# Kernel tuning notes

Measured on AMD Instinct MI355X. Metric: run time of the kernel, lower is better.

## Reference

```python
import jax, jax.numpy as jnp
import numpy as np

B, S, H, NH, FF, L = 2, 2048, 768, 12, 3072, 2
DH = H // NH
EPS = 1e-12
NEG = -10000.0


def setup_inputs() -> dict:
    key = jax.random.key(0)
    ks = jax.random.split(key, 10)
    w = lambda k, shp: jax.random.normal(k, shp, dtype=jnp.float32) * 0.02
    return {
        'hidden_states': jax.random.normal(ks[0], (B, S, H), dtype=jnp.float32),
        'attention_mask': jnp.ones((B, S), jnp.float32),
        'bias_matrix': jax.random.normal(ks[1], (S, S), dtype=jnp.float32) * 0.1,
        'bias_coef': jnp.ones((), jnp.float32),
        'Wq': w(ks[2], (L, H, H)), 'bq': jnp.zeros((L, H), jnp.float32),
        'Wk': w(ks[3], (L, H, H)), 'bk': jnp.zeros((L, H), jnp.float32),
        'Wv': w(ks[4], (L, H, H)), 'bv': jnp.zeros((L, H), jnp.float32),
        'Wo': w(ks[5], (L, H, H)), 'bo': jnp.zeros((L, H), jnp.float32),
        'ln1_g': jnp.ones((L, H), jnp.float32), 'ln1_b': jnp.zeros((L, H), jnp.float32),
        'Wi': w(ks[6], (L, H, FF)), 'bi': jnp.zeros((L, FF), jnp.float32),
        'Wo2': w(ks[7], (L, FF, H)), 'bo2': jnp.zeros((L, H), jnp.float32),
        'ln2_g': jnp.ones((L, H), jnp.float32), 'ln2_b': jnp.zeros((L, H), jnp.float32),
    }


def _layer_norm(x, g, b):
    mu = jnp.mean(x, axis=-1, keepdims=True)
    var = jnp.mean(jnp.square(x - mu), axis=-1, keepdims=True)
    return (x - mu) * jax.lax.rsqrt(var + EPS) * g + b


def reference(hidden_states, attention_mask, bias_matrix, bias_coef,
              Wq, bq, Wk, bk, Wv, bv, Wo, bo, ln1_g, ln1_b,
              Wi, bi, Wo2, bo2, ln2_g, ln2_b):
    # extended additive mask: [B,1,1,S]
    ext_mask = (1.0 - attention_mask)[:, None, None, :] * NEG
    bias = bias_matrix[None, None] * bias_coef  # [1,1,S,S]
    x = hidden_states
    scale = 1.0 / np.sqrt(DH)
    for i in range(L):
        q = (x @ Wq[i] + bq[i]).reshape(B, S, NH, DH).transpose(0, 2, 1, 3)
        k = (x @ Wk[i] + bk[i]).reshape(B, S, NH, DH).transpose(0, 2, 1, 3)
        v = (x @ Wv[i] + bv[i]).reshape(B, S, NH, DH).transpose(0, 2, 1, 3)
        scores = jnp.einsum('bhqd,bhkd->bhqk', q, k) * scale
        scores = scores + bias + ext_mask
        probs = jax.nn.softmax(scores, axis=-1)  # dropout = identity (eval)
        ctx = jnp.einsum('bhqk,bhkd->bhqd', probs, v)
        ctx = ctx.transpose(0, 2, 1, 3).reshape(B, S, H)
        attn_out = ctx @ Wo[i] + bo[i]
        x = _layer_norm(attn_out + x, ln1_g[i], ln1_b[i])
        inter = jax.nn.gelu(x @ Wi[i] + bi[i], approximate=False)
        ffn_out = inter @ Wo2[i] + bo2[i]
        x = _layer_norm(ffn_out + x, ln2_g[i], ln2_b[i])
    return x
```

## Files before the change

### kernel.cpp

```cpp
#include <hip/hip_runtime.h>
#include <hip/hip_bf16.h>
#include <math.h>

#define BB     2
#define SS     2048
#define HH     768
#define NHEAD  12
#define DHEAD  64
#define FFD    3072
#define NLAYER 2
#define MTOK   (BB*SS)

typedef __attribute__((ext_vector_type(8))) short bf16x8;
typedef __attribute__((ext_vector_type(4))) short bf16x4;
typedef __attribute__((ext_vector_type(4))) float f32x4;

__device__ __forceinline__ short f2bs(float f) {
    union { float f; unsigned u; } v; v.f = f;
    unsigned r = v.u + 0x7FFF + ((v.u >> 16) & 1);
    return (short)(r >> 16);
}
__device__ __forceinline__ float bs2f(short s) {
    union { unsigned u; float f; } v; v.u = ((unsigned)(unsigned short)s) << 16;
    return v.f;
}
__device__ __forceinline__ void gl2lds16(const short* g, short* l) {
    __builtin_amdgcn_global_load_lds(
        (const __attribute__((address_space(1))) unsigned int*)g,
        (__attribute__((address_space(3))) unsigned int*)l, 16, 0, 0);
}

struct TJobs { const float* src[8]; short* dst[8]; };

__global__ __launch_bounds__(256)
void transpose_cvt_batch(TJobs jobs, int K, int N)
{
    const float* __restrict__ W  = jobs.src[blockIdx.z];
    short* __restrict__ Wt = jobs.dst[blockIdx.z];
    __shared__ short tile[32][33];
    const int k0 = blockIdx.x * 32, n0 = blockIdx.y * 32;
    const int tx = threadIdx.x & 31, ty = threadIdx.x >> 5;
#pragma unroll
    for (int i = 0; i < 4; i++)
        tile[ty + i*8][tx] = f2bs(W[(size_t)(k0 + ty + i*8) * N + n0 + tx]);
    __syncthreads();
#pragma unroll
    for (int i = 0; i < 4; i++)
        Wt[(size_t)(n0 + ty + i*8) * K + k0 + tx] = tile[tx][ty + i*8];
}

__global__ __launch_bounds__(256)
void cvt_bf16(const float* __restrict__ src, short* __restrict__ dst, int n)
{
    const int i = blockIdx.x * 256 + threadIdx.x;
    if (i < n) dst[i] = f2bs(src[i]);
}

__global__ __launch_bounds__(256)
void pack_bias(const float* __restrict__ bq, const float* __restrict__ bk,
               const float* __restrict__ bv, float* __restrict__ bqkv)
{
    const int t = blockIdx.x * 256 + threadIdx.x;
    if (t >= NLAYER * 2304) return;
    const int l = t / 2304, r = t % 2304;
    const float* src = (r < 768) ? bq : (r < 1536 ? bk : bv);
    bqkv[t] = src[l*768 + (r % 768)];
}

__global__ __launch_bounds__(256)
void bias_frag_prep(const float* __restrict__ biasM, const float* __restrict__ mask,
                    const float* __restrict__ coefp, short* __restrict__ bFrag)
{
    __shared__ float tile[64][129];
    const int tid = threadIdx.x;
    const int qb = blockIdx.x, q0 = qb*64, k0 = blockIdx.y*128;
#pragma unroll
    for (int p = 0; p < 8; p++) {
        const int row = p*8 + (tid >> 5);
        const int col = (tid & 31) * 4;
        float4 v = *(const float4*)&biasM[(size_t)(q0 + row)*SS + k0 + col];
        tile[row][col+0] = v.x; tile[row][col+1] = v.y;
        tile[row][col+2] = v.z; tile[row][col+3] = v.w;
    }
    __syncthreads();
    const float coef = coefp[0];
    const int lane = tid & 63, w = tid >> 6;
    const int l16 = lane & 15, g = lane >> 4;
    const int qrow = w*16 + l16;
#pragma unroll
    for (int b = 0; b < BB; b++) {
#pragma unroll
        for (int kt = 0; kt < 8; kt++) {
            bf16x4 o;
#pragma unroll
            for (int r = 0; r < 4; r++) {
                const int kk = kt*16 + g*4 + r;
                const float madd = (1.f - mask[b*SS + k0 + kk]) * (-10000.0f);
                o[r] = f2bs(tile[qrow][kk] * coef + madd);
            }
            const size_t idx = ((((size_t)b*32 + qb)*4 + w)*128 + (k0>>4) + kt)*256 + lane*4;
            *(bf16x4*)&bFrag[idx] = o;
        }
    }
}

__global__ __launch_bounds__(256)
void gemm_mfma(const short* __restrict__ A, const short* __restrict__ Bt,
               const float* __restrict__ bias, short* __restrict__ C, int ldc,
               int M, int N, int K, int gelu, short* __restrict__ VtOut, int vsplit)
{
    __shared__ short sA[128*32];
    __shared__ short sB[128*32];
    const int tid  = threadIdx.x;
    const int w    = tid >> 6;
    const int lane = tid & 63;
    const int l16  = lane & 15, g = lane >> 4;
    const int wm   = w & 1, wn = w >> 1;
    const size_t m0 = (size_t)blockIdx.y * 128, n0 = (size_t)blockIdx.x * 128;

    const int srow = lane >> 2;
    const int kc   = lane & 3;

    f32x4 acc[4][4];
#pragma unroll
    for (int i = 0; i < 4; i++)
#pragma unroll
        for (int j = 0; j < 4; j++) acc[i][j] = (f32x4){0.f,0.f,0.f,0.f};

    const short* gA0 = A  + (m0 + w*32 +      srow) * (size_t)K + kc*8;
    const short* gA1 = A  + (m0 + w*32 + 16 + srow) * (size_t)K + kc*8;
    const short* gB0 = Bt + (n0 + w*32 +      srow) * (size_t)K + kc*8;
    const short* gB1 = Bt + (n0 + w*32 + 16 + srow) * (size_t)K + kc*8;
    short* lA0 = &sA[(w*32     )*32];
    short* lA1 = &sA[(w*32 + 16)*32];
    short* lB0 = &sB[(w*32     )*32];
    short* lB1 = &sB[(w*32 + 16)*32];

    for (int k0 = 0; k0 < K; k0 += 32) {
        gl2lds16(gA0 + k0, lA0);
        gl2lds16(gA1 + k0, lA1);
        gl2lds16(gB0 + k0, lB0);
        gl2lds16(gB1 + k0, lB1);
        __syncthreads();

        bf16x8 af[4], bfr[4];
#pragma unroll
        for (int mt = 0; mt < 4; mt++)
            af[mt] = *(const bf16x8*)&sA[(wm*64 + mt*16 + l16)*32 + g*8];
#pragma unroll
        for (int nt = 0; nt < 4; nt++)
            bfr[nt] = *(const bf16x8*)&sB[(wn*64 + nt*16 + l16)*32 + g*8];
#pragma unroll
        for (int mt = 0; mt < 4; mt++)
#pragma unroll
            for (int nt = 0; nt < 4; nt++)
                acc[mt][nt] = __builtin_amdgcn_mfma_f32_16x16x32_bf16(
                                  af[mt], bfr[nt], acc[mt][nt], 0, 0, 0);
        __syncthreads();
    }

#pragma unroll
    for (int mt = 0; mt < 4; mt++) {
        const size_t row0 = m0 + wm*64 + mt*16 + g*4;
#pragma unroll
        for (int nt = 0; nt < 4; nt++) {
            const size_t col = n0 + wn*64 + nt*16 + l16;
            if ((int)col >= vsplit) {
                short4 t;
                t.x = f2bs(acc[mt][nt][0] + bias[col]);
                t.y = f2bs(acc[mt][nt][1] + bias[col]);
                t.z = f2bs(acc[mt][nt][2] + bias[col]);
                t.w = f2bs(acc[mt][nt][3] + bias[col]);
                *(short4*)&VtOut[(size_t)(col - vsplit)*MTOK + row0] = t;
            } else {
#pragma unroll
                for (int r = 0; r < 4; r++) {
                    float v = acc[mt][nt][r] + bias[col];
                    if (gelu) v = 0.5f * v * (1.f + erff(v * 0.70710678118f));
                    C[(row0 + r) * (size_t)ldc + col] = f2bs(v);
                }
            }
        }
    }
}

__global__ __launch_bounds__(256)
void gemm_mfma_n64(const short* __restrict__ A, const short* __restrict__ Bt,
                   const float* __restrict__ bias, short* __restrict__ C, int ldc,
                   int M, int N, int K, int gelu)
{
    __shared__ short sA[128*32];
    __shared__ short sB[64*32];
    const int tid  = threadIdx.x;
    const int w    = tid >> 6;
    const int lane = tid & 63;
    const int l16  = lane & 15, g = lane >> 4;
    const int wm   = w & 1, wn = w >> 1;
    const size_t m0 = (size_t)blockIdx.y * 128, n0 = (size_t)blockIdx.x * 64;

    const int srow = lane >> 2;
    const int kc   = lane & 3;

    f32x4 acc[4][2];
#pragma unroll
    for (int i = 0; i < 4; i++)
#pragma unroll
        for (int j = 0; j < 2; j++) acc[i][j] = (f32x4){0.f,0.f,0.f,0.f};

    const short* gA0 = A  + (m0 + w*32 +      srow) * (size_t)K + kc*8;
    const short* gA1 = A  + (m0 + w*32 + 16 + srow) * (size_t)K + kc*8;
    const short* gB0 = Bt + (n0 + w*16 +      srow) * (size_t)K + kc*8;
    short* lA0 = &sA[(w*32     )*32];
    short* lA1 = &sA[(w*32 + 16)*32];
    short* lB0 = &sB[(w*16     )*32];

    for (int k0 = 0; k0 < K; k0 += 32) {
        gl2lds16(gA0 + k0, lA0);
        gl2lds16(gA1 + k0, lA1);
        gl2lds16(gB0 + k0, lB0);
        __syncthreads();

        bf16x8 af[4], bfr[2];
#pragma unroll
        for (int mt = 0; mt < 4; mt++)
            af[mt] = *(const bf16x8*)&sA[(wm*64 + mt*16 + l16)*32 + g*8];
#pragma unroll
        for (int nt = 0; nt < 2; nt++)
            bfr[nt] = *(const bf16x8*)&sB[(wn*32 + nt*16 + l16)*32 + g*8];
#pragma unroll
        for (int mt = 0; mt < 4; mt++)
#pragma unroll
            for (int nt = 0; nt < 2; nt++)
                acc[mt][nt] = __builtin_amdgcn_mfma_f32_16x16x32_bf16(
                                  af[mt], bfr[nt], acc[mt][nt], 0, 0, 0);
        __syncthreads();
    }

#pragma unroll
    for (int mt = 0; mt < 4; mt++) {
        const size_t row0 = m0 + wm*64 + mt*16 + g*4;
#pragma unroll
        for (int nt = 0; nt < 2; nt++) {
            const size_t col = n0 + wn*32 + nt*16 + l16;
#pragma unroll
            for (int r = 0; r < 4; r++) {
                float v = acc[mt][nt][r] + bias[col];
                if (gelu) v = 0.5f * v * (1.f + erff(v * 0.70710678118f));
                C[(row0 + r) * (size_t)ldc + col] = f2bs(v);
            }
        }
    }
}

__global__ __launch_bounds__(256, 3)
void attn_fused(const short* __restrict__ QK, const short* __restrict__ Vt,
                const short* __restrict__ bFrag, short* __restrict__ CTX)
{
    __shared__ short sK[128*72];
    __shared__ short sV[64*136];
    __shared__ short sP[64*136];

    const int qb  = blockIdx.x;
    const int q0  = qb * 64;
    const int h   = blockIdx.y;
    const int b   = blockIdx.z;
    const int tid = threadIdx.x;
    const int w   = tid >> 6;
    const int lane = tid & 63;
    const int l16 = lane & 15;
    const int g   = lane >> 4;
    const float scale = 0.125f;

    const short* qrow = QK + ((size_t)(b*SS) + q0 + w*16 + l16) * 1536 + h*64;
    bf16x8 bQ0 = *(const bf16x8*)(qrow + g*8);
    bf16x8 bQ1 = *(const bf16x8*)(qrow + 32 + g*8);

    f32x4 O[4];
#pragma unroll
    for (int d = 0; d < 4; d++) O[d] = (f32x4){0.f,0.f,0.f,0.f};
    float m_q = -1e30f, l_q = 0.f;

    const int krow = tid >> 3, kch = tid & 7;
    const int vrow = tid >> 4, vch = tid & 15;
    const short* Kg = QK + ((size_t)(b*SS) + krow)*1536 + 768 + h*64 + kch*8;
    const short* Vg = Vt + ((size_t)(h*64 + vrow))*MTOK + b*SS + vch*8;
    const short* bF = bFrag + ((((size_t)b*32 + qb)*4 + w)*128)*256 + lane*4;

    short* prow = &sP[(w*16 + l16)*136];

    bf16x8 kreg[4], vreg[4];
#pragma unroll
    for (int p = 0; p < 4; p++) {
        kreg[p] = *(const bf16x8*)(Kg + (size_t)(p*32)*1536);
        vreg[p] = *(const bf16x8*)(Vg + (size_t)(p*16)*MTOK);
    }

    for (int k0 = 0; k0 < SS; k0 += 128) {
        const short* bFt = bF + ((size_t)(k0 >> 4))*256;
        bf16x4 bb[8];
#pragma unroll
        for (int t = 0; t < 8; t++)
            bb[t] = *(const bf16x4*)(bFt + (size_t)t*256);

#pragma unroll
        for (int p = 0; p < 4; p++) {
            *(bf16x8*)&sK[(p*32 + krow)*72 + kch*8]   = kreg[p];
            *(bf16x8*)&sV[(p*16 + vrow)*136 + vch*8]  = vreg[p];
        }
        __syncthreads();

        if (k0 + 128 < SS) {
#pragma unroll
            for (int p = 0; p < 4; p++) {
                kreg[p] = *(const bf16x8*)(Kg + (size_t)(k0 + 128 + p*32)*1536);
                vreg[p] = *(const bf16x8*)(Vg + (size_t)(p*16)*MTOK + k0 + 128);
            }
        }

        float S[8][4];
#pragma unroll
        for (int t = 0; t < 8; t++) {
            bf16x8 aK0 = *(const bf16x8*)&sK[(t*16 + l16)*72 + g*8];
            bf16x8 aK1 = *(const bf16x8*)&sK[(t*16 + l16)*72 + 32 + g*8];
            f32x4 c = (f32x4){0.f,0.f,0.f,0.f};
            c = __builtin_amdgcn_mfma_f32_16x16x32_bf16(aK0, bQ0, c, 0, 0, 0);
            c = __builtin_amdgcn_mfma_f32_16x16x32_bf16(aK1, bQ1, c, 0, 0, 0);
#pragma unroll
            for (int r = 0; r < 4; r++)
                S[t][r] = c[r]*scale + bs2f(bb[t][r]);
        }

        float tm[8];
#pragma unroll
        for (int t = 0; t < 8; t++)
            tm[t] = fmaxf(fmaxf(S[t][0], S[t][1]), fmaxf(S[t][2], S[t][3]));
        float mx = fmaxf(fmaxf(fmaxf(tm[0], tm[1]), fmaxf(tm[2], tm[3])),
                         fmaxf(fmaxf(tm[4], tm[5]), fmaxf(tm[6], tm[7])));
        mx = fmaxf(mx, __shfl_xor(mx, 16));
        mx = fmaxf(mx, __shfl_xor(mx, 32));
        const float mnew  = fmaxf(m_q, mx);
        const float alpha = __expf(m_q - mnew);
        float ts[8];
#pragma unroll
        for (int t = 0; t < 8; t++) {
            float p0 = __expf(S[t][0] - mnew);
            float p1 = __expf(S[t][1] - mnew);
            float p2 = __expf(S[t][2] - mnew);
            float p3 = __expf(S[t][3] - mnew);
            S[t][0] = p0; S[t][1] = p1; S[t][2] = p2; S[t][3] = p3;
            ts[t] = (p0 + p1) + (p2 + p3);
        }
        float rs = ((ts[0] + ts[1]) + (ts[2] + ts[3]))
                 + ((ts[4] + ts[5]) + (ts[6] + ts[7]));
        rs += __shfl_xor(rs, 16);
        rs += __shfl_xor(rs, 32);
        l_q = l_q * alpha + rs;
        m_q = mnew;

#pragma unroll
        for (int r = 0; r < 4; r++) {
            const float ar = __shfl(alpha, g*4 + r);
#pragma unroll
            for (int d = 0; d < 4; d++) O[d][r] *= ar;
        }

#pragma unroll
        for (int t = 0; t < 8; t++) {
            unsigned int d0, d1;
            asm("v_cvt_pk_bf16_f32 %0, %1, %2" : "=v"(d0) : "v"(S[t][0]), "v"(S[t][1]));
            asm("v_cvt_pk_bf16_f32 %0, %1, %2" : "=v"(d1) : "v"(S[t][2]), "v"(S[t][3]));
            uint2 u; u.x = d0; u.y = d1;
            *(uint2*)&prow[t*16 + g*4] = u;
        }

#pragma unroll
        for (int hh = 0; hh < 2; hh++) {
            bf16x8 aP0 = *(const bf16x8*)&prow[hh*64 + g*8];
            bf16x8 aP1 = *(const bf16x8*)&prow[hh*64 + 32 + g*8];
#pragma unroll
            for (int d = 0; d < 4; d++) {
                bf16x8 v0 = *(const bf16x8*)&sV[(d*16 + l16)*136 + hh*64 + g*8];
                bf16x8 v1 = *(const bf16x8*)&sV[(d*16 + l16)*136 + hh*64 + 32 + g*8];
                O[d] = __builtin_amdgcn_mfma_f32_16x16x32_bf16(aP0, v0, O[d], 0, 0, 0);
                O[d] = __builtin_amdgcn_mfma_f32_16x16x32_bf16(aP1, v1, O[d], 0, 0, 0);
            }
        }
        __syncthreads();
    }

    float linv[4];
#pragma unroll
    for (int r = 0; r < 4; r++)
        linv[r] = 1.f / __shfl(l_q, g*4 + r);
#pragma unroll
    for (int d = 0; d < 4; d++)
#pragma unroll
        for (int r = 0; r < 4; r++)
            CTX[((size_t)(b*SS) + q0 + w*16 + g*4 + r)*HH + h*64 + d*16 + l16]
                = f2bs(O[d][r] * linv[r]);
}

__global__ __launch_bounds__(256)
void add_ln(const short* __restrict__ A, const short* __restrict__ R,
            const float* __restrict__ g, const float* __restrict__ beta,
            short* __restrict__ Out, float* __restrict__ OutF)
{
    const int lane = threadIdx.x & 63;
    const int row  = blockIdx.x * 4 + (threadIdx.x >> 6);
    const size_t base = (size_t)row * HH;

    float v[12];
    float s = 0.f;
#pragma unroll
    for (int p = 0; p < 3; p++) {
        const int c = p*256 + lane*4;
        bf16x4 av = *(const bf16x4*)&A[base + c];
        bf16x4 rv = *(const bf16x4*)&R[base + c];
#pragma unroll
        for (int j = 0; j < 4; j++) {
            float x = bs2f(av[j]) + bs2f(rv[j]);
            v[p*4 + j] = x;
            s += x;
        }
    }
    s += __shfl_xor(s, 1);  s += __shfl_xor(s, 2);  s += __shfl_xor(s, 4);
    s += __shfl_xor(s, 8);  s += __shfl_xor(s, 16); s += __shfl_xor(s, 32);
    const float mu = s * (1.f / HH);

    float s2 = 0.f;
#pragma unroll
    for (int j = 0; j < 12; j++) { float d = v[j] - mu; s2 += d * d; }
    s2 += __shfl_xor(s2, 1);  s2 += __shfl_xor(s2, 2);  s2 += __shfl_xor(s2, 4);
    s2 += __shfl_xor(s2, 8);  s2 += __shfl_xor(s2, 16); s2 += __shfl_xor(s2, 32);
    const float rstd = rsqrtf(s2 * (1.f / HH) + 1e-12f);

#pragma unroll
    for (int p = 0; p < 3; p++) {
        const int c = p*256 + lane*4;
        float4 gv = *(const float4*)&g[c];
        float4 bv = *(const float4*)&beta[c];
        float o0 = (v[p*4+0] - mu) * rstd * gv.x + bv.x;
        float o1 = (v[p*4+1] - mu) * rstd * gv.y + bv.y;
        float o2 = (v[p*4+2] - mu) * rstd * gv.z + bv.z;
        float o3 = (v[p*4+3] - mu) * rstd * gv.w + bv.w;
        bf16x4 ov; ov[0] = f2bs(o0); ov[1] = f2bs(o1); ov[2] = f2bs(o2); ov[3] = f2bs(o3);
        *(bf16x4*)&Out[base + c] = ov;
        if (OutF) {
            float4 of; of.x = o0; of.y = o1; of.z = o2; of.w = o3;
            *(float4*)&OutF[base + c] = of;
        }
    }
}

extern "C" void kernel_launch(void* const* d_in, const int* in_sizes, int n_in,
                              void* d_out, int out_size, void* d_ws, size_t ws_size,
                              hipStream_t stream)
{
    const float* hs    = (const float*)d_in[0];
    const float* mask  = (const float*)d_in[1];
    const float* biasM = (const float*)d_in[2];
    const float* coef  = (const float*)d_in[3];
    const float* Wq    = (const float*)d_in[4];
    const float* bq    = (const float*)d_in[5];
    const float* Wk    = (const float*)d_in[6];
    const float* bk    = (const float*)d_in[7];
    const float* Wv    = (const float*)d_in[8];
    const float* bv    = (const float*)d_in[9];
    const float* Wo    = (const float*)d_in[10];
    const float* bo    = (const float*)d_in[11];
    const float* ln1g  = (const float*)d_in[12];
    const float* ln1b  = (const float*)d_in[13];
    const float* Wi    = (const float*)d_in[14];
    const float* bi    = (const float*)d_in[15];
    const float* Wo2   = (const float*)d_in[16];
    const float* bo2   = (const float*)d_in[17];
    const float* ln2g  = (const float*)d_in[18];
    const float* ln2b  = (const float*)d_in[19];

    const size_t sH   = (size_t)MTOK * HH;
    const size_t sQK  = (size_t)MTOK * 1536;
    const size_t sVt  = (size_t)HH * MTOK;
    const size_t WPL  = 7077888;
    short* wt    = (short*)d_ws;
    float* bqkv  = (float*)(wt + 2*WPL);
    short* bFrag = (short*)(bqkv + 2*2304);
    short* X     = bFrag + (size_t)2*SS*SS;
    short* X2    = X  + sH;
    short* QK    = X2 + sH;
    short* Vt    = QK + sQK;
    short* CTX   = Vt + sVt;
    short* TMP   = QK;
    short* INTER = QK;
    short* TMP2  = X;

    const dim3 blk(256);

    TJobs jH, jI, jO;
    for (int l = 0; l < NLAYER; l++) {
        short* wl = wt + (size_t)l * WPL;
        jH.src[l*4+0] = Wq + (size_t)l*HH*HH;  jH.dst[l*4+0] = wl;
        jH.src[l*4+1] = Wk + (size_t)l*HH*HH;  jH.dst[l*4+1] = wl + 768*768;
        jH.src[l*4+2] = Wv + (size_t)l*HH*HH;  jH.dst[l*4+2] = wl + 1536*768;
        jH.src[l*4+3] = Wo + (size_t)l*HH*HH;  jH.dst[l*4+3] = wl + 1769472;
        jI.src[l] = Wi  + (size_t)l*HH*FFD;    jI.dst[l] = wl + 2359296;
        jO.src[l] = Wo2 + (size_t)l*FFD*HH;    jO.dst[l] = wl + 4718592;
    }
    transpose_cvt_batch<<<dim3(24,24,8), blk, 0, stream>>>(jH, HH, HH);
    transpose_cvt_batch<<<dim3(24,96,2), blk, 0, stream>>>(jI, HH, FFD);
    transpose_cvt_batch<<<dim3(96,24,2), blk, 0, stream>>>(jO, FFD, HH);
    bias_frag_prep<<<dim3(SS/64, SS/128), blk, 0, stream>>>(biasM, mask, coef, bFrag);
    pack_bias<<<dim3((NLAYER*2304 + 255)/256), blk, 0, stream>>>(bq, bk, bv, bqkv);
    cvt_bf16<<<dim3((int)((sH + 255)/256)), blk, 0, stream>>>(hs, X, (int)sH);

    const dim3 gQKV(2304/128, MTOK/128);
    const dim3 gH64(HH/64,    MTOK/128);
    const dim3 gFF (FFD/128,  MTOK/128);
    const dim3 gA  (SS/64, NHEAD, BB);
    const dim3 gLN (MTOK/4);
    const int NOSPLIT = 1 << 30;

    for (int l = 0; l < NLAYER; l++) {
        short* wl = wt + (size_t)l * WPL;
        gemm_mfma<<<gQKV, blk, 0, stream>>>(X, wl, bqkv + l*2304, QK, 1536,
                                            MTOK, 2304, HH, 0, Vt, 1536);
        attn_fused<<<gA, blk, 0, stream>>>(QK, Vt, bFrag, CTX);
        gemm_mfma_n64<<<gH64, blk, 0, stream>>>(CTX, wl + 1769472, bo + l*HH, TMP, HH,
                                                MTOK, HH, HH, 0);
        add_ln<<<gLN, blk, 0, stream>>>(TMP, X, ln1g + l*HH, ln1b + l*HH, X2, nullptr);
        gemm_mfma<<<gFF, blk, 0, stream>>>(X2, wl + 2359296, bi + l*FFD, INTER, FFD,
                                           MTOK, FFD, HH, 1, nullptr, NOSPLIT);
        gemm_mfma_n64<<<gH64, blk, 0, stream>>>(INTER, wl + 4718592, bo2 + l*HH, TMP2, HH,
                                                MTOK, HH, FFD, 0);
        add_ln<<<gLN, blk, 0, stream>>>(TMP2, X2, ln2g + l*HH, ln2b + l*HH, X,
                                        (l == NLAYER-1) ? (float*)d_out : nullptr);
    }
}
```

Measured before the change: 604.9 us.

## Keep P in registers via permlane swaps, load V directly from global, double-buffer K

The attention kernel no longer stages P and V through shared memory. The softmax probabilities are repacked in registers with v_permlane32/16_swap into the MFMA operand layout, and V fragments are loaded straight from global memory in matching layout, split into two batches to overlap with the softmax math. K tiles are double-buffered in LDS so there is one barrier per iteration. This cuts LDS traffic and footprint, which may allow higher occupancy, but relies on permlane swap semantics being correct and adds global-load latency for V on the critical path.

```diff
diff --git a/kernel.cpp b/kernel.cpp
--- a/kernel.cpp
+++ b/kernel.cpp
@@ -256,9 +256,7 @@
 void attn_fused(const short* __restrict__ QK, const short* __restrict__ Vt,
                 const short* __restrict__ bFrag, short* __restrict__ CTX)
 {
-    __shared__ short sK[128*72];
-    __shared__ short sV[64*136];
-    __shared__ short sP[64*136];
+    __shared__ short sK[2][128*72];
 
     const int qb  = blockIdx.x;
     const int q0  = qb * 64;
@@ -281,53 +279,62 @@
     float m_q = -1e30f, l_q = 0.f;
 
     const int krow = tid >> 3, kch = tid & 7;
-    const int vrow = tid >> 4, vch = tid & 15;
     const short* Kg = QK + ((size_t)(b*SS) + krow)*1536 + 768 + h*64 + kch*8;
-    const short* Vg = Vt + ((size_t)(h*64 + vrow))*MTOK + b*SS + vch*8;
+    const short* Vg = Vt + ((size_t)(h*64 + l16))*MTOK + b*SS + g*8;
     const short* bF = bFrag + ((((size_t)b*32 + qb)*4 + w)*128)*256 + lane*4;
 
-    short* prow = &sP[(w*16 + l16)*136];
-
-    bf16x8 kreg[4], vreg[4];
-#pragma unroll
-    for (int p = 0; p < 4; p++) {
+    bf16x8 kreg[4];
+#pragma unroll
+    for (int p = 0; p < 4; p++)
         kreg[p] = *(const bf16x8*)(Kg + (size_t)(p*32)*1536);
-        vreg[p] = *(const bf16x8*)(Vg + (size_t)(p*16)*MTOK);
-    }
+#pragma unroll
+    for (int p = 0; p < 4; p++)
+        *(bf16x8*)&sK[0][(p*32 + krow)*72 + kch*8] = kreg[p];
+#pragma unroll
+    for (int p = 0; p < 4; p++)
+        kreg[p] = *(const bf16x8*)(Kg + (size_t)(128 + p*32)*1536);
+    __syncthreads();
 
     for (int k0 = 0; k0 < SS; k0 += 128) {
+        const int cur = (k0 >> 7) & 1;
+        const short* sKc = sK[cur];
+
+        if (k0 + 128 < SS) {
+            short* sKn = sK[cur ^ 1];
+#pragma unroll
+            for (int p = 0; p < 4; p++)
+                *(bf16x8*)&sKn[(p*32 + krow)*72 + kch*8] = kreg[p];
+            if (k0 + 256 < SS) {
+#pragma unroll
+                for (int p = 0; p < 4; p++)
+                    kreg[p] = *(const bf16x8*)(Kg + (size_t)(k0 + 256 + p*32)*1536);
+            }
+        }
+
         const short* bFt = bF + ((size_t)(k0 >> 4))*256;
         bf16x4 bb[8];
 #pragma unroll
         for (int t = 0; t < 8; t++)
             bb[t] = *(const bf16x4*)(bFt + (size_t)t*256);
 
-#pragma unroll
-        for (int p = 0; p < 4; p++) {
-            *(bf16x8*)&sK[(p*32 + krow)*72 + kch*8]   = kreg[p];
-            *(bf16x8*)&sV[(p*16 + vrow)*136 + vch*8]  = vreg[p];
-        }
-        __syncthreads();
-
-        if (k0 + 128 < SS) {
-#pragma unroll
-            for (int p = 0; p < 4; p++) {
-                kreg[p] = *(const bf16x8*)(Kg + (size_t)(k0 + 128 + p*32)*1536);
-                vreg[p] = *(const bf16x8*)(Vg + (size_t)(p*16)*MTOK + k0 + 128);
-            }
-        }
-
         float S[8][4];
 #pragma unroll
         for (int t = 0; t < 8; t++) {
-            bf16x8 aK0 = *(const bf16x8*)&sK[(t*16 + l16)*72 + g*8];
-            bf16x8 aK1 = *(const bf16x8*)&sK[(t*16 + l16)*72 + 32 + g*8];
+            bf16x8 aK0 = *(const bf16x8*)&sKc[(t*16 + l16)*72 + g*8];
+            bf16x8 aK1 = *(const bf16x8*)&sKc[(t*16 + l16)*72 + 32 + g*8];
             f32x4 c = (f32x4){0.f,0.f,0.f,0.f};
             c = __builtin_amdgcn_mfma_f32_16x16x32_bf16(aK0, bQ0, c, 0, 0, 0);
             c = __builtin_amdgcn_mfma_f32_16x16x32_bf16(aK1, bQ1, c, 0, 0, 0);
 #pragma unroll
             for (int r = 0; r < 4; r++)
                 S[t][r] = c[r]*scale + bs2f(bb[t][r]);
+        }
+
+        bf16x8 vf0[4], vf1[4];
+#pragma unroll
+        for (int d = 0; d < 4; d++) {
+            vf0[d] = *(const bf16x8*)(Vg + (size_t)(d*16)*MTOK + k0);
+            vf1[d] = *(const bf16x8*)(Vg + (size_t)(d*16)*MTOK + k0 + 32);
         }
 
         float tm[8];
@@ -357,6 +364,13 @@
         l_q = l_q * alpha + rs;
         m_q = mnew;
 
+        bf16x8 vf2[4], vf3[4];
+#pragma unroll
+        for (int d = 0; d < 4; d++) {
+            vf2[d] = *(const bf16x8*)(Vg + (size_t)(d*16)*MTOK + k0 + 64);
+            vf3[d] = *(const bf16x8*)(Vg + (size_t)(d*16)*MTOK + k0 + 96);
+        }
+
 #pragma unroll
         for (int r = 0; r < 4; r++) {
             const float ar = __shfl(alpha, g*4 + r);
@@ -364,27 +378,34 @@
             for (int d = 0; d < 4; d++) O[d][r] *= ar;
         }
 
-#pragma unroll
-        for (int t = 0; t < 8; t++) {
-            unsigned int d0, d1;
-            asm("v_cvt_pk_bf16_f32 %0, %1, %2" : "=v"(d0) : "v"(S[t][0]), "v"(S[t][1]));
-            asm("v_cvt_pk_bf16_f32 %0, %1, %2" : "=v"(d1) : "v"(S[t][2]), "v"(S[t][3]));
-            uint2 u; u.x = d0; u.y = d1;
-            *(uint2*)&prow[t*16 + g*4] = u;
-        }
-
-#pragma unroll
-        for (int hh = 0; hh < 2; hh++) {
-            bf16x8 aP0 = *(const bf16x8*)&prow[hh*64 + g*8];
-            bf16x8 aP1 = *(const bf16x8*)&prow[hh*64 + 32 + g*8];
-#pragma unroll
-            for (int d = 0; d < 4; d++) {
-                bf16x8 v0 = *(const bf16x8*)&sV[(d*16 + l16)*136 + hh*64 + g*8];
-                bf16x8 v1 = *(const bf16x8*)&sV[(d*16 + l16)*136 + hh*64 + 32 + g*8];
-                O[d] = __builtin_amdgcn_mfma_f32_16x16x32_bf16(aP0, v0, O[d], 0, 0, 0);
-                O[d] = __builtin_amdgcn_mfma_f32_16x16x32_bf16(aP1, v1, O[d], 0, 0, 0);
-            }
-        }
+#define PVU(u, vf)                                                             \
+        {                                                                      \
+            unsigned pa, pb, pc, pe;                                           \
+            asm("v_cvt_pk_bf16_f32 %0, %1, %2" : "=v"(pa)                      \
+                : "v"(S[2*(u)][0]),   "v"(S[2*(u)][1]));                       \
+            asm("v_cvt_pk_bf16_f32 %0, %1, %2" : "=v"(pb)                      \
+                : "v"(S[2*(u)][2]),   "v"(S[2*(u)][3]));                       \
+            asm("v_cvt_pk_bf16_f32 %0, %1, %2" : "=v"(pc)                      \
+                : "v"(S[2*(u)+1][0]), "v"(S[2*(u)+1][1]));                     \
+            asm("v_cvt_pk_bf16_f32 %0, %1, %2" : "=v"(pe)                      \
+                : "v"(S[2*(u)+1][2]), "v"(S[2*(u)+1][3]));                     \
+            asm("v_permlane32_swap_b32 %0, %1" : "+v"(pa), "+v"(pc));          \
+            asm("v_permlane16_swap_b32 %0, %1" : "+v"(pa), "+v"(pc));          \
+            asm("v_permlane32_swap_b32 %0, %1" : "+v"(pb), "+v"(pe));          \
+            asm("v_permlane16_swap_b32 %0, %1" : "+v"(pb), "+v"(pe));          \
+            union { unsigned uw[4]; bf16x8 v; } P_;                            \
+            P_.uw[0] = pa; P_.uw[1] = pb; P_.uw[2] = pc; P_.uw[3] = pe;        \
+            _Pragma("unroll")                                                  \
+            for (int d = 0; d < 4; d++)                                        \
+                O[d] = __builtin_amdgcn_mfma_f32_16x16x32_bf16(                \
+                           P_.v, vf[d], O[d], 0, 0, 0);                        \
+        }
+        PVU(0, vf0)
+        PVU(1, vf1)
+        PVU(2, vf2)
+        PVU(3, vf3)
+#undef PVU
+
         __syncthreads();
     }
 
```

Result: slower. 705.6 us (+16.6%).

## Use K=64 tiles in GEMMs and register-permute P for attention PV

Applied to the files above, without the earlier changes.

Both GEMM kernels now stage two 32-wide K slices per iteration into doubled shared buffers, which halves the number of barrier pairs per K sweep at the cost of more LDS per block. The attention kernel no longer writes softmax probabilities to shared memory and reads them back. It converts them to bf16 and rearranges them across lanes with permlane swap instructions to form the MFMA A operand directly. That removes the sP buffer, and the launch bound rises to 4 blocks per CU. The lane permutation has to match the MFMA operand layout exactly, and the higher occupancy target can constrain register allocation.

```diff
diff --git a/kernel.cpp b/kernel.cpp
--- a/kernel.cpp
+++ b/kernel.cpp
@@ -109,8 +109,8 @@
                const float* __restrict__ bias, short* __restrict__ C, int ldc,
                int M, int N, int K, int gelu, short* __restrict__ VtOut, int vsplit)
 {
-    __shared__ short sA[128*32];
-    __shared__ short sB[128*32];
+    __shared__ short sA[2][128*32];
+    __shared__ short sB[2][128*32];
     const int tid  = threadIdx.x;
     const int w    = tid >> 6;
     const int lane = tid & 63;
@@ -131,31 +131,35 @@
     const short* gA1 = A  + (m0 + w*32 + 16 + srow) * (size_t)K + kc*8;
     const short* gB0 = Bt + (n0 + w*32 +      srow) * (size_t)K + kc*8;
     const short* gB1 = Bt + (n0 + w*32 + 16 + srow) * (size_t)K + kc*8;
-    short* lA0 = &sA[(w*32     )*32];
-    short* lA1 = &sA[(w*32 + 16)*32];
-    short* lB0 = &sB[(w*32     )*32];
-    short* lB1 = &sB[(w*32 + 16)*32];
-
-    for (int k0 = 0; k0 < K; k0 += 32) {
-        gl2lds16(gA0 + k0, lA0);
-        gl2lds16(gA1 + k0, lA1);
-        gl2lds16(gB0 + k0, lB0);
-        gl2lds16(gB1 + k0, lB1);
+    const int oA0 = (w*32     )*32, oA1 = (w*32 + 16)*32;
+
+    for (int k0 = 0; k0 < K; k0 += 64) {
+        gl2lds16(gA0 + k0,      &sA[0][oA0]);
+        gl2lds16(gA1 + k0,      &sA[0][oA1]);
+        gl2lds16(gB0 + k0,      &sB[0][oA0]);
+        gl2lds16(gB1 + k0,      &sB[0][oA1]);
+        gl2lds16(gA0 + k0 + 32, &sA[1][oA0]);
+        gl2lds16(gA1 + k0 + 32, &sA[1][oA1]);
+        gl2lds16(gB0 + k0 + 32, &sB[1][oA0]);
+        gl2lds16(gB1 + k0 + 32, &sB[1][oA1]);
         __syncthreads();
 
-        bf16x8 af[4], bfr[4];
-#pragma unroll
-        for (int mt = 0; mt < 4; mt++)
-            af[mt] = *(const bf16x8*)&sA[(wm*64 + mt*16 + l16)*32 + g*8];
-#pragma unroll
-        for (int nt = 0; nt < 4; nt++)
-            bfr[nt] = *(const bf16x8*)&sB[(wn*64 + nt*16 + l16)*32 + g*8];
-#pragma unroll
-        for (int mt = 0; mt < 4; mt++)
+#pragma unroll
+        for (int s = 0; s < 2; s++) {
+            bf16x8 af[4], bfr[4];
+#pragma unroll
+            for (int mt = 0; mt < 4; mt++)
+                af[mt] = *(const bf16x8*)&sA[s][(wm*64 + mt*16 + l16)*32 + g*8];
 #pragma unroll
             for (int nt = 0; nt < 4; nt++)
-                acc[mt][nt] = __builtin_amdgcn_mfma_f32_16x16x32_bf16(
-                                  af[mt], bfr[nt], acc[mt][nt], 0, 0, 0);
+                bfr[nt] = *(const bf16x8*)&sB[s][(wn*64 + nt*16 + l16)*32 + g*8];
+#pragma unroll
+            for (int mt = 0; mt < 4; mt++)
+#pragma unroll
+                for (int nt = 0; nt < 4; nt++)
+                    acc[mt][nt] = __builtin_amdgcn_mfma_f32_16x16x32_bf16(
+                                      af[mt], bfr[nt], acc[mt][nt], 0, 0, 0);
+        }
         __syncthreads();
     }
 
@@ -189,8 +193,8 @@
                    const float* __restrict__ bias, short* __restrict__ C, int ldc,
                    int M, int N, int K, int gelu)
 {
-    __shared__ short sA[128*32];
-    __shared__ short sB[64*32];
+    __shared__ short sA[2][128*32];
+    __shared__ short sB[2][64*32];
     const int tid  = threadIdx.x;
     const int w    = tid >> 6;
     const int lane = tid & 63;
@@ -210,29 +214,33 @@
     const short* gA0 = A  + (m0 + w*32 +      srow) * (size_t)K + kc*8;
     const short* gA1 = A  + (m0 + w*32 + 16 + srow) * (size_t)K + kc*8;
     const short* gB0 = Bt + (n0 + w*16 +      srow) * (size_t)K + kc*8;
-    short* lA0 = &sA[(w*32     )*32];
-    short* lA1 = &sA[(w*32 + 16)*32];
-    short* lB0 = &sB[(w*16     )*32];
-
-    for (int k0 = 0; k0 < K; k0 += 32) {
-        gl2lds16(gA0 + k0, lA0);
-        gl2lds16(gA1 + k0, lA1);
-        gl2lds16(gB0 + k0, lB0);
+    const int oA0 = (w*32     )*32, oA1 = (w*32 + 16)*32, oB0 = (w*16)*32;
+
+    for (int k0 = 0; k0 < K; k0 += 64) {
+        gl2lds16(gA0 + k0,      &sA[0][oA0]);
+        gl2lds16(gA1 + k0,      &sA[0][oA1]);
+        gl2lds16(gB0 + k0,      &sB[0][oB0]);
+        gl2lds16(gA0 + k0 + 32, &sA[1][oA0]);
+        gl2lds16(gA1 + k0 + 32, &sA[1][oA1]);
+        gl2lds16(gB0 + k0 + 32, &sB[1][oB0]);
         __syncthreads();
 
-        bf16x8 af[4], bfr[2];
-#pragma unroll
-        for (int mt = 0; mt < 4; mt++)
-            af[mt] = *(const bf16x8*)&sA[(wm*64 + mt*16 + l16)*32 + g*8];
-#pragma unroll
-        for (int nt = 0; nt < 2; nt++)
-            bfr[nt] = *(const bf16x8*)&sB[(wn*32 + nt*16 + l16)*32 + g*8];
-#pragma unroll
-        for (int mt = 0; mt < 4; mt++)
+#pragma unroll
+        for (int s = 0; s < 2; s++) {
+            bf16x8 af[4], bfr[2];
+#pragma unroll
+            for (int mt = 0; mt < 4; mt++)
+                af[mt] = *(const bf16x8*)&sA[s][(wm*64 + mt*16 + l16)*32 + g*8];
 #pragma unroll
             for (int nt = 0; nt < 2; nt++)
-                acc[mt][nt] = __builtin_amdgcn_mfma_f32_16x16x32_bf16(
-                                  af[mt], bfr[nt], acc[mt][nt], 0, 0, 0);
+                bfr[nt] = *(const bf16x8*)&sB[s][(wn*32 + nt*16 + l16)*32 + g*8];
+#pragma unroll
+            for (int mt = 0; mt < 4; mt++)
+#pragma unroll
+                for (int nt = 0; nt < 2; nt++)
+                    acc[mt][nt] = __builtin_amdgcn_mfma_f32_16x16x32_bf16(
+                                      af[mt], bfr[nt], acc[mt][nt], 0, 0, 0);
+        }
         __syncthreads();
     }
 
@@ -252,13 +260,12 @@
     }
 }
 
-__global__ __launch_bounds__(256, 3)
+__global__ __launch_bounds__(256, 4)
 void attn_fused(const short* __restrict__ QK, const short* __restrict__ Vt,
                 const short* __restrict__ bFrag, short* __restrict__ CTX)
 {
     __shared__ short sK[128*72];
     __shared__ short sV[64*136];
-    __shared__ short sP[64*136];
 
     const int qb  = blockIdx.x;
     const int q0  = qb * 64;
@@ -286,8 +293,6 @@
     const short* Vg = Vt + ((size_t)(h*64 + vrow))*MTOK + b*SS + vch*8;
     const short* bF = bFrag + ((((size_t)b*32 + qb)*4 + w)*128)*256 + lane*4;
 
-    short* prow = &sP[(w*16 + l16)*136];
-
     bf16x8 kreg[4], vreg[4];
 #pragma unroll
     for (int p = 0; p < 4; p++) {
@@ -364,27 +369,36 @@
             for (int d = 0; d < 4; d++) O[d][r] *= ar;
         }
 
-#pragma unroll
-        for (int t = 0; t < 8; t++) {
-            unsigned int d0, d1;
-            asm("v_cvt_pk_bf16_f32 %0, %1, %2" : "=v"(d0) : "v"(S[t][0]), "v"(S[t][1]));
-            asm("v_cvt_pk_bf16_f32 %0, %1, %2" : "=v"(d1) : "v"(S[t][2]), "v"(S[t][3]));
-            uint2 u; u.x = d0; u.y = d1;
-            *(uint2*)&prow[t*16 + g*4] = u;
-        }
-
-#pragma unroll
-        for (int hh = 0; hh < 2; hh++) {
-            bf16x8 aP0 = *(const bf16x8*)&prow[hh*64 + g*8];
-            bf16x8 aP1 = *(const bf16x8*)&prow[hh*64 + 32 + g*8];
-#pragma unroll
-            for (int d = 0; d < 4; d++) {
-                bf16x8 v0 = *(const bf16x8*)&sV[(d*16 + l16)*136 + hh*64 + g*8];
-                bf16x8 v1 = *(const bf16x8*)&sV[(d*16 + l16)*136 + hh*64 + 32 + g*8];
-                O[d] = __builtin_amdgcn_mfma_f32_16x16x32_bf16(aP0, v0, O[d], 0, 0, 0);
-                O[d] = __builtin_amdgcn_mfma_f32_16x16x32_bf16(aP1, v1, O[d], 0, 0, 0);
-            }
-        }
+#define PVU(u)                                                                 \
+        {                                                                      \
+            unsigned pa, pb, pc, pe;                                           \
+            asm("v_cvt_pk_bf16_f32 %0, %1, %2" : "=v"(pa)                      \
+                : "v"(S[2*(u)][0]),   "v"(S[2*(u)][1]));                       \
+            asm("v_cvt_pk_bf16_f32 %0, %1, %2" : "=v"(pb)                      \
+                : "v"(S[2*(u)][2]),   "v"(S[2*(u)][3]));                       \
+            asm("v_cvt_pk_bf16_f32 %0, %1, %2" : "=v"(pc)                      \
+                : "v"(S[2*(u)+1][0]), "v"(S[2*(u)+1][1]));                     \
+            asm("v_cvt_pk_bf16_f32 %0, %1, %2" : "=v"(pe)                      \
+                : "v"(S[2*(u)+1][2]), "v"(S[2*(u)+1][3]));                     \
+            asm("v_permlane32_swap_b32 %0, %1" : "+v"(pa), "+v"(pc));          \
+            asm("v_permlane16_swap_b32 %0, %1" : "+v"(pa), "+v"(pc));          \
+            asm("v_permlane32_swap_b32 %0, %1" : "+v"(pb), "+v"(pe));          \
+            asm("v_permlane16_swap_b32 %0, %1" : "+v"(pb), "+v"(pe));          \
+            union { unsigned uw[4]; bf16x8 v; } P_;                            \
+            P_.uw[0] = pa; P_.uw[1] = pb; P_.uw[2] = pc; P_.uw[3] = pe;        \
+            _Pragma("unroll")                                                  \
+            for (int d = 0; d < 4; d++) {                                      \
+                bf16x8 vv = *(const bf16x8*)&sV[(d*16 + l16)*136 + (u)*32 + g*8]; \
+                O[d] = __builtin_amdgcn_mfma_f32_16x16x32_bf16(                \
+                           P_.v, vv, O[d], 0, 0, 0);                           \
+            }                                                                  \
+        }
+        PVU(0)
+        PVU(1)
+        PVU(2)
+        PVU(3)
+#undef PVU
+
         __syncthreads();
     }
 
```

Result: faster. 573.5 us (-5.2%).
